# Performance work log

Hardware: AMD Instinct MI355X
Metric: run time of the kernel (lower is better)

Reference implementation:

```python
import jax, jax.numpy as jnp
import numpy as np

ALPHA = 2.0  # spikingjelly surrogate.ATan default alpha

@jax.custom_vjp
def spike(x):
    # IFNode firing: Heaviside(v - v_threshold) with v_reset=0 and single-step reset,
    # so output = H(x) where x = input - v_threshold.
    return (x >= 0.0).astype(x.dtype)

def _spike_fwd(x):
    return spike(x), x

def _spike_bwd(x, g):
    # ATan surrogate gradient: alpha/2 / (1 + (pi/2 * alpha * x)^2)
    s = (jnp.pi / 2.0) * ALPHA * x
    return (g * (ALPHA / 2.0) / (1.0 + s * s),)

spike.defvjp(_spike_fwd, _spike_bwd)

def setup_inputs() -> dict:
    key = jax.random.key(0)
    batch, T = 16384, 2048
    u = jax.random.uniform(key, (batch, T), dtype=jnp.float32)
    spike_train = (u < 0.1).astype(jnp.float32)
    return {"spike_train": spike_train}

def reference(spike_train):
    # first_spike[t] = AND(spike[t], NOT(prev_any)); prev_any = OR(prev_any, spike[t])
    # AND: H(a+b-1.5); OR: H(a+b-0.5); NOT: H(1-a-0.5)
    def step(prev_any, cur):
        not_prev = spike(1.0 - prev_any - 0.5)          # NOTGate
        first = spike(cur + not_prev - 1.5)              # ANDGate
        new_prev = spike(prev_any + cur - 0.5)           # ORGate
        return new_prev, first

    batch = spike_train.shape[0]
    prev0 = jnp.zeros((batch,), dtype=spike_train.dtype)
    # scan over time axis: inputs [T, batch]
    _, firsts = jax.lax.scan(step, prev0, spike_train.T)
    return firsts.T  # [batch, T]
```

## Files before the change

kernel.cpp:

```cpp
#include <hip/hip_runtime.h>
#include <climits>


__global__ __launch_bounds__(256, 1) void first_spike_kernel(
    const float* __restrict__ in, float* __restrict__ out, int batch, int T) {
  const int lane = threadIdx.x & 63;
  const int wave = threadIdx.x >> 6;
  const int row  = blockIdx.x * 4 + wave;
  if (row >= batch) return;

  const float4* __restrict__ in4  = (const float4*)(in  + (size_t)row * T);
  float4*       __restrict__ out4 = (float4*)      (out + (size_t)row * T);
  const int iters = T >> 8;

  int first_idx = INT_MAX;
  for (int it = 0; it < iters; ++it) {
    float4 v = in4[(it << 6) + lane];
    const int base = (it << 8) + (lane << 2);
    int local = INT_MAX;
    if (v.w != 0.0f) local = base + 3;
    if (v.z != 0.0f) local = base + 2;
    if (v.y != 0.0f) local = base + 1;
    if (v.x != 0.0f) local = base + 0;
    if (__ballot(local != INT_MAX)) {
      int m = local;
#pragma unroll
      for (int off = 1; off < 64; off <<= 1)
        m = min(m, __shfl_xor(m, off, 64));
      first_idx = m;
      break;
    }
  }

#pragma unroll
  for (int it = 0; it < iters; ++it) {
    const int base = (it << 8) + (lane << 2);
    float4 o;
    o.x = (base + 0 == first_idx) ? 1.0f : 0.0f;
    o.y = (base + 1 == first_idx) ? 1.0f : 0.0f;
    o.z = (base + 2 == first_idx) ? 1.0f : 0.0f;
    o.w = (base + 3 == first_idx) ? 1.0f : 0.0f;
    out4[(it << 6) + lane] = o;
  }
}

extern "C" void kernel_launch(void* const* d_in, const int* in_sizes, int n_in,
                              void* d_out, int out_size, void* d_ws, size_t ws_size,
                              hipStream_t stream) {
  const float* in = (const float*)d_in[0];
  float* out = (float*)d_out;
  const int T = 2048;
  const int batch = in_sizes[0] / T;
  const int waves_per_block = 4;
  dim3 grid((batch + waves_per_block - 1) / waves_per_block);
  first_spike_kernel<<<grid, 256, 0, stream>>>(in, out, batch, T);
}
```

Before: 202.2 us.

## Zero output with memset and scatter only the first-spike index per row

Replaces the dense per-row output write with an async memset of the whole output followed by a kernel that scans each row with scalar loads and a ballot, then writes a single 1.0 at the first spike position. It also raises the occupancy hint in launch bounds. The aim is to offload the bulk zero fill to the memset path, which may write faster than the kernel's stores. The cost is an extra serialized operation, and the scan now reads with scalar rather than vector loads.

```diff
diff --git a/kernel.cpp b/kernel.cpp
--- a/kernel.cpp
+++ b/kernel.cpp
@@ -1,46 +1,26 @@
 #include <hip/hip_runtime.h>
-#include <climits>
 
 
-__global__ __launch_bounds__(256, 1) void first_spike_kernel(
+__global__ __launch_bounds__(256, 4) void first_spike_scatter(
     const float* __restrict__ in, float* __restrict__ out, int batch, int T) {
   const int lane = threadIdx.x & 63;
   const int wave = threadIdx.x >> 6;
   const int row  = blockIdx.x * 4 + wave;
   if (row >= batch) return;
 
-  const float4* __restrict__ in4  = (const float4*)(in  + (size_t)row * T);
-  float4*       __restrict__ out4 = (float4*)      (out + (size_t)row * T);
-  const int iters = T >> 8;
+  const float* __restrict__ rowp = in + (size_t)row * T;
+  const int iters = T >> 6;
 
-  int first_idx = INT_MAX;
   for (int it = 0; it < iters; ++it) {
-    float4 v = in4[(it << 6) + lane];
-    const int base = (it << 8) + (lane << 2);
-    int local = INT_MAX;
-    if (v.w != 0.0f) local = base + 3;
-    if (v.z != 0.0f) local = base + 2;
-    if (v.y != 0.0f) local = base + 1;
-    if (v.x != 0.0f) local = base + 0;
-    if (__ballot(local != INT_MAX)) {
-      int m = local;
-#pragma unroll
-      for (int off = 1; off < 64; off <<= 1)
-        m = min(m, __shfl_xor(m, off, 64));
-      first_idx = m;
-      break;
+    float v = rowp[(it << 6) + lane];
+    unsigned long long mask = __ballot(v != 0.0f);
+    if (mask) {
+      if (lane == 0) {
+        int idx = (it << 6) + (__ffsll(mask) - 1);
+        out[(size_t)row * T + idx] = 1.0f;
+      }
+      return;
     }
-  }
-
-#pragma unroll
-  for (int it = 0; it < iters; ++it) {
-    const int base = (it << 8) + (lane << 2);
-    float4 o;
-    o.x = (base + 0 == first_idx) ? 1.0f : 0.0f;
-    o.y = (base + 1 == first_idx) ? 1.0f : 0.0f;
-    o.z = (base + 2 == first_idx) ? 1.0f : 0.0f;
-    o.w = (base + 3 == first_idx) ? 1.0f : 0.0f;
-    out4[(it << 6) + lane] = o;
   }
 }
 
@@ -51,7 +31,10 @@
   float* out = (float*)d_out;
   const int T = 2048;
   const int batch = in_sizes[0] / T;
+
+  hipMemsetAsync(d_out, 0, (size_t)out_size * sizeof(float), stream);
+
   const int waves_per_block = 4;
   dim3 grid((batch + waves_per_block - 1) / waves_per_block);
-  first_spike_kernel<<<grid, 256, 0, stream>>>(in, out, batch, T);
+  first_spike_scatter<<<grid, 256, 0, stream>>>(in, out, batch, T);
 }
```

New measurement: 200.1 us. Within noise of the previous version (-1.0%).
